# Kernel optimization log

Hardware: AMD Instinct MI355X
Metric: run time of the kernel (lower is better)

Reference implementation:

```python
import jax, jax.numpy as jnp
import numpy as np

B, N, C, R, E = 8, 4096, 128, 16, 65536


def setup_inputs() -> dict:
    key = jax.random.key(0)
    ks = jax.random.split(key, 8)
    node_features = jax.random.normal(ks[0], (B, N, C), dtype=jnp.float32)
    edge_index = jax.random.randint(ks[1], (B, 2, E), 0, N, dtype=jnp.int64)
    edge_type = jax.random.randint(ks[2], (B, E), 0, R, dtype=jnp.int64)
    s = 1.0 / np.sqrt(C)
    rel_weight = jax.random.uniform(ks[3], (R, C, C), jnp.float32, -s, s)
    root_weight = jax.random.uniform(ks[4], (C, C), jnp.float32, -s, s)
    rgcn_bias = jnp.zeros((C,), jnp.float32)
    lin_weight = jax.random.uniform(ks[5], (C, 1), jnp.float32, -s, s)
    lin_bias = jnp.zeros((1,), jnp.float32)
    return {
        'node_features': node_features,
        'edge_index': edge_index,
        'edge_type': edge_type,
        'rel_weight': rel_weight,
        'root_weight': root_weight,
        'rgcn_bias': rgcn_bias,
        'lin_weight': lin_weight,
        'lin_bias': lin_bias,
    }


def _rgcn_score(node_features, edge_index, edge_type, rel_weight, root_weight,
                rgcn_bias, lin_weight, lin_bias):
    # Flatten batch of graphs into one big disjoint graph (as batch_rgcn does).
    x = node_features.reshape(B * N, C)
    offs = (jnp.arange(B, dtype=edge_index.dtype) * N)[:, None, None]  # (B,1,1)
    ei = (edge_index + offs).transpose(1, 0, 2).reshape(2, B * E)  # (2, B*E)
    et = edge_type.reshape(B * E)
    src, dst = ei[0], ei[1]

    x_src = x[src]  # (B*E, C) gathered source features
    # root transform + bias (RGCNConv root_weight + bias)
    out = x @ root_weight + rgcn_bias  # (B*N, C)
    # per-relation mean aggregation; mean(W_r x_j) == W_r mean(x_j)
    for r in range(R):
        mask = (et == r).astype(x.dtype)  # (B*E,)
        s = jax.ops.segment_sum(x_src * mask[:, None], dst, num_segments=B * N)
        cnt = jax.ops.segment_sum(mask, dst, num_segments=B * N)
        mean = jnp.where(cnt[:, None] > 0, s / jnp.maximum(cnt, 1.0)[:, None], 0.0)
        out = out + mean @ rel_weight[r]

    out = jax.nn.relu(out)  # dropout is identity at eval
    scores = (out @ lin_weight + lin_bias).reshape(B, N)
    return scores


def reference(node_features, edge_index, edge_type, rel_weight, root_weight,
              rgcn_bias, lin_weight, lin_bias):
    return _rgcn_score(node_features, edge_index, edge_type, rel_weight,
                       root_weight, rgcn_bias, lin_weight, lin_bias)
```

## Files before the change

kernel.cpp:

```cpp
#include <hip/hip_runtime.h>

#define BB 8
#define NN 4096
#define CC 128
#define RR 16
#define EE 65536
#define NNODES 32768
#define NEDGES 524288
#define KTOT   2176
#define LDP    80
#define CSP    136
#define BCAP   60
#define GEMMB  4352
#define EDGEB  2048

typedef unsigned short ushort_t;
typedef short bf16x8 __attribute__((ext_vector_type(8)));
typedef float f32x4 __attribute__((ext_vector_type(4)));

__device__ __forceinline__ unsigned short f2b(float f) {
    unsigned u = __builtin_bit_cast(unsigned, f);
    unsigned r = (u + 0x7fffu + ((u >> 16) & 1u)) >> 16;
    return (unsigned short)r;
}
__device__ __forceinline__ float b2f(unsigned short s) {
    return __builtin_bit_cast(float, (unsigned)s << 16);
}
__device__ __forceinline__ float ldf(const void* p, int j, int isbf) {
    return isbf ? b2f(((const ushort_t*)p)[j]) : ((const float*)p)[j];
}
__device__ __forceinline__ int ldi(const int* p, int j, int is64) {
    return p[j << is64];
}

__device__ __forceinline__ int probe_isbf(const ushort_t* xf) {
    int t = threadIdx.x & 63;
    int bad = 0;
    for (int j = t; j < 512; j += 64) {
        unsigned e = (xf[j] >> 7) & 0xffu;
        if (e >= 160u) bad = 1;
    }
    return __ballot(bad) == 0ull;
}

__global__ __launch_bounds__(256) void prep_k(const void* __restrict__ x,
                                              const void* __restrict__ relw,
                                              const void* __restrict__ rootw,
                                              const int* __restrict__ ei,
                                              const int* __restrict__ et,
                                              ushort_t* __restrict__ Xb,
                                              ushort_t* __restrict__ WT,
                                              int* __restrict__ dcnt,
                                              int* __restrict__ flags) {
    int bx = blockIdx.x, t = threadIdx.x;
    if (bx < 2048) {
        int isbf = probe_isbf((const ushort_t*)x);
        int tid = bx * 256 + t;
        if (isbf) {
            ((uint4*)Xb)[tid] = ((const uint4*)x)[tid];
        } else {
            const float4* xf = (const float4*)x;
            float4 a = xf[2 * tid], b = xf[2 * tid + 1];
            ushort4 o0, o1;
            o0.x = f2b(a.x); o0.y = f2b(a.y); o0.z = f2b(a.z); o0.w = f2b(a.w);
            o1.x = f2b(b.x); o1.y = f2b(b.y); o1.z = f2b(b.z); o1.w = f2b(b.w);
            ((ushort4*)Xb)[2 * tid] = o0; ((ushort4*)Xb)[2 * tid + 1] = o1;
        }
    } else if (bx < 3136) {
        int isbf = probe_isbf((const ushort_t*)x);
        int tid = (bx - 2048) * 256 + t;
        int nglob = tid >> 7, k = tid & 127;
        int jb = nglob >> 7, n = nglob & 127;
        float v = (jb == 0) ? ldf(rootw, k * 128 + n, isbf)
                            : ldf(relw, ((jb - 1) << 14) + k * 128 + n, isbf);
        WT[tid] = f2b(v);
    } else if (bx < 3168) {
        int tid = (bx - 3136) * 256 + t;
        ((uint4*)dcnt)[tid] = make_uint4(0, 0, 0, 0);
    } else {
        if (t < 64) {
            int isbf = probe_isbf((const ushort_t*)x);
            int a = (t < 16) ? ei[2 * t + 1] : 0;
            int b = (t < 16) ? et[2 * t + 1] : 0;
            unsigned long long ma = __ballot(a != 0);
            unsigned long long mb = __ballot(b != 0);
            if (t == 0) {
                flags[0] = isbf;
                flags[1] = (ma == 0ull);
                flags[2] = (mb == 0ull);
            }
        }
    }
}

__global__ __launch_bounds__(256) void ge_k(const ushort_t* __restrict__ Xb,
                                            const ushort_t* __restrict__ WT,
                                            ushort_t* __restrict__ Y,
                                            const int* __restrict__ ei,
                                            const int* __restrict__ et,
                                            int* __restrict__ dcnt,
                                            int* __restrict__ bucket,
                                            const int* __restrict__ flags) {
    __shared__ ushort_t smem[2 * 128 * LDP];
    int bx = blockIdx.x, t = threadIdx.x;
    if (bx < EDGEB) {
        int w64i = flags[1], w64t = flags[2];
        int tid = bx * 256 + t;
        int b = tid >> 16, e = tid & 65535;
        int src = ldi(ei, (b * 2) * EE + e, w64i);
        int dst = ldi(ei, (b * 2 + 1) * EE + e, w64i);
        int r = ldi(et, tid, w64t);
        int gd = (b << 12) + dst;
        int pos = atomicAdd(&dcnt[gd], 1);
        if (pos < BCAP)
            bucket[gd * BCAP + pos] = (((b << 12) + src) << 4) | r;
        return;
    }
    int bxg = bx - EDGEB;
    ushort_t* As = smem;
    ushort_t* Bs = smem + 128 * LDP;
    int m0 = (bxg & 255) * 128, n0 = (bxg >> 8) * 128;
    int wave = t >> 6, lane = t & 63, lrow = lane & 15, lq = lane >> 4;
    int wm = (wave >> 1) * 64, wn = (wave & 1) * 64;
    f32x4 acc[4][4] = {};

    for (int kt = 0; kt < 2; ++kt) {
        #pragma unroll
        for (int i = 0; i < 4; ++i) {
            int c = t + i * 256;
            int row = c >> 3, c8 = c & 7;
            uint4 va = *(const uint4*)(Xb + (size_t)(m0 + row) * 128 + kt * 64 + c8 * 8);
            *(uint4*)(&As[row * LDP + c8 * 8]) = va;
            uint4 vb = *(const uint4*)(WT + (size_t)(n0 + row) * 128 + kt * 64 + c8 * 8);
            *(uint4*)(&Bs[row * LDP + c8 * 8]) = vb;
        }
        __syncthreads();
        #pragma unroll
        for (int ks = 0; ks < 2; ++ks) {
            int k0 = ks * 32 + lq * 8;
            bf16x8 a[4], b[4];
            #pragma unroll
            for (int mi = 0; mi < 4; ++mi) a[mi] = *(const bf16x8*)(&As[(wm + mi * 16 + lrow) * LDP + k0]);
            #pragma unroll
            for (int ni = 0; ni < 4; ++ni) b[ni] = *(const bf16x8*)(&Bs[(wn + ni * 16 + lrow) * LDP + k0]);
            #pragma unroll
            for (int mi = 0; mi < 4; ++mi)
                #pragma unroll
                for (int ni = 0; ni < 4; ++ni)
                    acc[mi][ni] = __builtin_amdgcn_mfma_f32_16x16x32_bf16(a[mi], b[ni], acc[mi][ni], 0, 0, 0);
        }
        __syncthreads();
    }
    ushort_t* Cs = smem;
    #pragma unroll
    for (int mi = 0; mi < 4; ++mi)
        #pragma unroll
        for (int rg = 0; rg < 4; ++rg) {
            int row = wm + mi * 16 + lq * 4 + rg;
            #pragma unroll
            for (int ni = 0; ni < 4; ++ni)
                Cs[row * CSP + wn + ni * 16 + lrow] = f2b(acc[mi][ni][rg]);
        }
    __syncthreads();
    #pragma unroll
    for (int i = 0; i < 8; ++i) {
        int c = t + i * 256;
        int row = c >> 4, c16 = c & 15;
        uint4 v = *(const uint4*)(&Cs[row * CSP + c16 * 8]);
        *(uint4*)(Y + (size_t)(m0 + row) * KTOT + n0 + c16 * 8) = v;
    }
}

__global__ __launch_bounds__(128) void agg_score_k(const ushort_t* __restrict__ Y,
                                                   const int* __restrict__ dcnt,
                                                   const int* __restrict__ bucket,
                                                   const void* __restrict__ bias,
                                                   const void* __restrict__ linw,
                                                   const void* __restrict__ linb,
                                                   void* __restrict__ out,
                                                   const int* __restrict__ flags) {
    int i = blockIdx.x, t = threadIdx.x;
    int isbf = flags[0];
    __shared__ int scnt[RR];
    __shared__ float inv[RR];
    __shared__ int bke[64];
    __shared__ float part[128][9];
    int nc = dcnt[i]; if (nc > BCAP) nc = BCAP;
    const int* bk = bucket + i * BCAP;
    if (t < RR) scnt[t] = 0;
    __syncthreads();
    if (t < nc) { int v = bk[t]; bke[t] = v; atomicAdd(&scnt[v & 15], 1); }
    __syncthreads();
    if (t < RR) inv[t] = (scnt[t] > 0) ? 1.0f / (float)scnt[t] : 0.0f;
    __syncthreads();

    int g = t >> 4, l16 = t & 15;
    float a8[8] = {};
    for (int base = 0; base < nc; base += 8) {
        int e = base + g;
        if (e < nc) {
            int v = bke[e];
            const ushort_t* yr = Y + (size_t)(v >> 4) * KTOT + CC + ((v & 15) << 7) + l16 * 8;
            uint4 u = *(const uint4*)yr;
            float w = inv[v & 15];
            a8[0] += w * __builtin_bit_cast(float, u.x << 16);
            a8[1] += w * __builtin_bit_cast(float, u.x & 0xffff0000u);
            a8[2] += w * __builtin_bit_cast(float, u.y << 16);
            a8[3] += w * __builtin_bit_cast(float, u.y & 0xffff0000u);
            a8[4] += w * __builtin_bit_cast(float, u.z << 16);
            a8[5] += w * __builtin_bit_cast(float, u.z & 0xffff0000u);
            a8[6] += w * __builtin_bit_cast(float, u.w << 16);
            a8[7] += w * __builtin_bit_cast(float, u.w & 0xffff0000u);
        }
    }
    #pragma unroll
    for (int j = 0; j < 8; ++j) part[l16 * 8 + j][g] = a8[j];
    __syncthreads();

    float acc = b2f(Y[(size_t)i * KTOT + t]) + ldf(bias, t, isbf);
    #pragma unroll
    for (int gg = 0; gg < 8; ++gg) acc += part[t][gg];
    float val = fmaxf(acc, 0.f) * ldf(linw, t, isbf);
    for (int o = 32; o > 0; o >>= 1) val += __shfl_down(val, o, 64);
    __shared__ float red[2];
    if ((t & 63) == 0) red[t >> 6] = val;
    __syncthreads();
    if (t == 0) {
        float res = red[0] + red[1] + ldf(linb, 0, isbf);
        if (isbf) ((ushort_t*)out)[i] = f2b(res);
        else      ((float*)out)[i] = res;
    }
}

extern "C" void kernel_launch(void* const* d_in, const int* in_sizes, int n_in,
                              void* d_out, int out_size, void* d_ws, size_t ws_size,
                              hipStream_t stream) {
    const void* x     = d_in[0];
    const int*  ei    = (const int*)d_in[1];
    const int*  et    = (const int*)d_in[2];
    const void* relw  = d_in[3];
    const void* rootw = d_in[4];
    const void* bias  = d_in[5];
    const void* linw  = d_in[6];
    const void* linb  = d_in[7];

    const size_t WS_NEED = 159547904;
    if (ws_size < WS_NEED) return;

    char* ws = (char*)d_ws;
    ushort_t* Y      = (ushort_t*)(ws);
    ushort_t* Xb     = (ushort_t*)(ws + 142606336);
    ushort_t* WT     = (ushort_t*)(ws + 150994944);
    int*      dcnt   = (int*)(ws + 151552000);
    int*      bucket = (int*)(ws + 151683072);
    int*      flags  = (int*)(ws + 159547392);

    prep_k<<<3169, 256, 0, stream>>>(x, relw, rootw, ei, et, Xb, WT, dcnt, flags);
    ge_k<<<EDGEB + GEMMB, 256, 0, stream>>>(Xb, WT, Y, ei, et, dcnt, bucket, flags);
    agg_score_k<<<NNODES, 128, 0, stream>>>(Y, dcnt, bucket, bias, linw, linb, d_out, flags);
}
```

Measured before the change: 167.1 us.

## Aggregate per relation first, then fuse concatenated GEMM with scoring

The algorithm changes from transform-then-gather to gather-then-transform. Before, a large Y = X·[root|W_r] table (32768×2176 bf16) was materialised and then gathered per edge. Now edges are bucketed by (dst, relation), and per-relation means of raw bf16 features are built in LDS for a 64-node tile. Those means are multiplied against a concatenated K=2176 weight with MFMA, and ReLU plus the linear score are fused into the epilogue. This removes the ~140MB Y write and re-read. The cost is a serial 17-pass loop per block, only 512 blocks, weights streamed straight from global memory, and a per-(node,relation) bucket capacity of 16 that could drop edges.

```diff
diff --git a/kernel.cpp b/kernel.cpp
--- a/kernel.cpp
+++ b/kernel.cpp
@@ -7,12 +7,10 @@
 #define EE 65536
 #define NNODES 32768
 #define NEDGES 524288
-#define KTOT   2176
-#define LDP    80
-#define CSP    136
-#define BCAP   60
-#define GEMMB  4352
-#define EDGEB  2048
+#define KW    2176
+#define SCAP  16
+#define NT    64
+#define ALP   136
 
 typedef unsigned short ushort_t;
 typedef short bf16x8 __attribute__((ext_vector_type(8)));
@@ -49,13 +47,28 @@
                                               const int* __restrict__ ei,
                                               const int* __restrict__ et,
                                               ushort_t* __restrict__ Xb,
-                                              ushort_t* __restrict__ WT,
-                                              int* __restrict__ dcnt,
+                                              ushort_t* __restrict__ WT2,
+                                              int* __restrict__ dcnt2,
+                                              int* __restrict__ bucket2,
                                               int* __restrict__ flags) {
     int bx = blockIdx.x, t = threadIdx.x;
     if (bx < 2048) {
+        int lane = t & 63;
+        int pa = (lane < 16) ? ei[2 * lane + 1] : 0;
+        int pb = (lane < 16) ? et[2 * lane + 1] : 0;
+        int w64i = (__ballot(pa != 0) == 0ull);
+        int w64t = (__ballot(pb != 0) == 0ull);
+        int tid = bx * 256 + t;
+        int b = tid >> 16, e = tid & 65535;
+        int src = ldi(ei, (b * 2) * EE + e, w64i);
+        int dst = ldi(ei, (b * 2 + 1) * EE + e, w64i);
+        int r = ldi(et, tid, w64t);
+        int key = (((b << 12) + dst) << 4) | r;
+        int pos = atomicAdd(&dcnt2[key], 1);
+        if (pos < SCAP) bucket2[key * SCAP + pos] = (b << 12) + src;
+    } else if (bx < 4096) {
         int isbf = probe_isbf((const ushort_t*)x);
-        int tid = bx * 256 + t;
+        int tid = (bx - 2048) * 256 + t;
         if (isbf) {
             ((uint4*)Xb)[tid] = ((const uint4*)x)[tid];
         } else {
@@ -66,169 +79,123 @@
             o1.x = f2b(b.x); o1.y = f2b(b.y); o1.z = f2b(b.z); o1.w = f2b(b.w);
             ((ushort4*)Xb)[2 * tid] = o0; ((ushort4*)Xb)[2 * tid + 1] = o1;
         }
-    } else if (bx < 3136) {
+    } else if (bx < 5184) {
         int isbf = probe_isbf((const ushort_t*)x);
-        int tid = (bx - 2048) * 256 + t;
-        int nglob = tid >> 7, k = tid & 127;
-        int jb = nglob >> 7, n = nglob & 127;
-        float v = (jb == 0) ? ldf(rootw, k * 128 + n, isbf)
-                            : ldf(relw, ((jb - 1) << 14) + k * 128 + n, isbf);
-        WT[tid] = f2b(v);
-    } else if (bx < 3168) {
-        int tid = (bx - 3136) * 256 + t;
-        ((uint4*)dcnt)[tid] = make_uint4(0, 0, 0, 0);
+        int tid = (bx - 4096) * 256 + t;
+        if (tid < 262144) {
+            int c = tid >> 11, kk = tid & 2047;
+            int r = kk >> 7, k = kk & 127;
+            WT2[c * KW + kk] = f2b(ldf(relw, (r << 14) + (k << 7) + c, isbf));
+        } else {
+            int t2 = tid - 262144;
+            int c = t2 >> 7, k = t2 & 127;
+            WT2[c * KW + 2048 + k] = f2b(ldf(rootw, (k << 7) + c, isbf));
+        }
     } else {
-        if (t < 64) {
-            int isbf = probe_isbf((const ushort_t*)x);
-            int a = (t < 16) ? ei[2 * t + 1] : 0;
-            int b = (t < 16) ? et[2 * t + 1] : 0;
-            unsigned long long ma = __ballot(a != 0);
-            unsigned long long mb = __ballot(b != 0);
-            if (t == 0) {
-                flags[0] = isbf;
-                flags[1] = (ma == 0ull);
-                flags[2] = (mb == 0ull);
+        int isbf = probe_isbf((const ushort_t*)x);
+        if (t == 0) flags[0] = isbf;
+    }
+}
+
+__global__ __launch_bounds__(256) void agg_k(const ushort_t* __restrict__ Xb,
+                                             const ushort_t* __restrict__ WT2,
+                                             const int* __restrict__ dcnt2,
+                                             const int* __restrict__ bucket2,
+                                             const void* __restrict__ bias,
+                                             const void* __restrict__ linw,
+                                             const void* __restrict__ linb,
+                                             void* __restrict__ out,
+                                             const int* __restrict__ flags) {
+    __shared__ ushort_t A[NT * ALP];
+    __shared__ int cnt[NT * 16];
+    __shared__ float red[NT][5];
+    int bx = blockIdx.x, t = threadIdx.x;
+    int isbf = flags[0];
+    int n0 = bx * NT;
+
+    #pragma unroll
+    for (int i = 0; i < 4; ++i) cnt[i * 256 + t] = dcnt2[n0 * 16 + i * 256 + t];
+
+    int nsub = t >> 2, tsub = t & 3;
+    int wave = t >> 6, lane = t & 63, lrow = lane & 15, lq = lane >> 4;
+    f32x4 acc[4][2] = {};
+
+    for (int pass = 0; pass < 17; ++pass) {
+        __syncthreads();
+        if (pass == 16) {
+            const uint4* s4 = (const uint4*)(Xb + (size_t)(n0 + nsub) * 128 + tsub * 32);
+            uint4* d4 = (uint4*)(&A[nsub * ALP + tsub * 32]);
+            #pragma unroll
+            for (int i = 0; i < 4; ++i) d4[i] = s4[i];
+        } else {
+            int cfull = cnt[nsub * 16 + pass];
+            int ce = cfull > SCAP ? SCAP : cfull;
+            float s[32];
+            #pragma unroll
+            for (int j = 0; j < 32; ++j) s[j] = 0.f;
+            const int* bk = bucket2 + ((size_t)(n0 + nsub) * 16 + pass) * SCAP;
+            for (int e2 = 0; e2 < ce; ++e2) {
+                int gs = bk[e2];
+                const unsigned* xr = (const unsigned*)(Xb + (size_t)gs * 128 + tsub * 32);
+                #pragma unroll
+                for (int j = 0; j < 16; ++j) {
+                    unsigned u = xr[j];
+                    s[2 * j]     += __builtin_bit_cast(float, u << 16);
+                    s[2 * j + 1] += __builtin_bit_cast(float, u & 0xffff0000u);
+                }
             }
-        }
-    }
-}
-
-__global__ __launch_bounds__(256) void ge_k(const ushort_t* __restrict__ Xb,
-                                            const ushort_t* __restrict__ WT,
-                                            ushort_t* __restrict__ Y,
-                                            const int* __restrict__ ei,
-                                            const int* __restrict__ et,
-                                            int* __restrict__ dcnt,
-                                            int* __restrict__ bucket,
-                                            const int* __restrict__ flags) {
-    __shared__ ushort_t smem[2 * 128 * LDP];
-    int bx = blockIdx.x, t = threadIdx.x;
-    if (bx < EDGEB) {
-        int w64i = flags[1], w64t = flags[2];
-        int tid = bx * 256 + t;
-        int b = tid >> 16, e = tid & 65535;
-        int src = ldi(ei, (b * 2) * EE + e, w64i);
-        int dst = ldi(ei, (b * 2 + 1) * EE + e, w64i);
-        int r = ldi(et, tid, w64t);
-        int gd = (b << 12) + dst;
-        int pos = atomicAdd(&dcnt[gd], 1);
-        if (pos < BCAP)
-            bucket[gd * BCAP + pos] = (((b << 12) + src) << 4) | r;
-        return;
-    }
-    int bxg = bx - EDGEB;
-    ushort_t* As = smem;
-    ushort_t* Bs = smem + 128 * LDP;
-    int m0 = (bxg & 255) * 128, n0 = (bxg >> 8) * 128;
-    int wave = t >> 6, lane = t & 63, lrow = lane & 15, lq = lane >> 4;
-    int wm = (wave >> 1) * 64, wn = (wave & 1) * 64;
-    f32x4 acc[4][4] = {};
-
-    for (int kt = 0; kt < 2; ++kt) {
+            float w = (cfull > 0) ? 1.0f / (float)cfull : 0.f;
+            uint4* d4 = (uint4*)(&A[nsub * ALP + tsub * 32]);
+            #pragma unroll
+            for (int i = 0; i < 4; ++i) {
+                uint4 v;
+                unsigned q0 = (unsigned)f2b(s[i * 8 + 0] * w) | ((unsigned)f2b(s[i * 8 + 1] * w) << 16);
+                unsigned q1 = (unsigned)f2b(s[i * 8 + 2] * w) | ((unsigned)f2b(s[i * 8 + 3] * w) << 16);
+                unsigned q2 = (unsigned)f2b(s[i * 8 + 4] * w) | ((unsigned)f2b(s[i * 8 + 5] * w) << 16);
+                unsigned q3 = (unsigned)f2b(s[i * 8 + 6] * w) | ((unsigned)f2b(s[i * 8 + 7] * w) << 16);
+                v.x = q0; v.y = q1; v.z = q2; v.w = q3;
+                d4[i] = v;
+            }
+        }
+        __syncthreads();
+        const ushort_t* bp0 = WT2 + (size_t)((wave * 2) * 16 + lrow) * KW + pass * 128;
+        const ushort_t* bp1 = bp0 + (size_t)16 * KW;
         #pragma unroll
-        for (int i = 0; i < 4; ++i) {
-            int c = t + i * 256;
-            int row = c >> 3, c8 = c & 7;
-            uint4 va = *(const uint4*)(Xb + (size_t)(m0 + row) * 128 + kt * 64 + c8 * 8);
-            *(uint4*)(&As[row * LDP + c8 * 8]) = va;
-            uint4 vb = *(const uint4*)(WT + (size_t)(n0 + row) * 128 + kt * 64 + c8 * 8);
-            *(uint4*)(&Bs[row * LDP + c8 * 8]) = vb;
-        }
-        __syncthreads();
-        #pragma unroll
-        for (int ks = 0; ks < 2; ++ks) {
+        for (int ks = 0; ks < 4; ++ks) {
             int k0 = ks * 32 + lq * 8;
-            bf16x8 a[4], b[4];
-            #pragma unroll
-            for (int mi = 0; mi < 4; ++mi) a[mi] = *(const bf16x8*)(&As[(wm + mi * 16 + lrow) * LDP + k0]);
-            #pragma unroll
-            for (int ni = 0; ni < 4; ++ni) b[ni] = *(const bf16x8*)(&Bs[(wn + ni * 16 + lrow) * LDP + k0]);
+            bf16x8 a[4], b0, b1;
             #pragma unroll
             for (int mi = 0; mi < 4; ++mi)
-                #pragma unroll
-                for (int ni = 0; ni < 4; ++ni)
-                    acc[mi][ni] = __builtin_amdgcn_mfma_f32_16x16x32_bf16(a[mi], b[ni], acc[mi][ni], 0, 0, 0);
-        }
-        __syncthreads();
-    }
-    ushort_t* Cs = smem;
+                a[mi] = *(const bf16x8*)(&A[(mi * 16 + lrow) * ALP + k0]);
+            b0 = *(const bf16x8*)(bp0 + k0);
+            b1 = *(const bf16x8*)(bp1 + k0);
+            #pragma unroll
+            for (int mi = 0; mi < 4; ++mi) {
+                acc[mi][0] = __builtin_amdgcn_mfma_f32_16x16x32_bf16(a[mi], b0, acc[mi][0], 0, 0, 0);
+                acc[mi][1] = __builtin_amdgcn_mfma_f32_16x16x32_bf16(a[mi], b1, acc[mi][1], 0, 0, 0);
+            }
+        }
+    }
+    int c0 = (wave * 2) * 16 + lrow, c1 = c0 + 16;
+    float bi0 = ldf(bias, c0, isbf), bi1 = ldf(bias, c1, isbf);
+    float lw0 = ldf(linw, c0, isbf), lw1 = ldf(linw, c1, isbf);
     #pragma unroll
     for (int mi = 0; mi < 4; ++mi)
         #pragma unroll
         for (int rg = 0; rg < 4; ++rg) {
-            int row = wm + mi * 16 + lq * 4 + rg;
-            #pragma unroll
-            for (int ni = 0; ni < 4; ++ni)
-                Cs[row * CSP + wn + ni * 16 + lrow] = f2b(acc[mi][ni][rg]);
+            float p = fmaxf(acc[mi][0][rg] + bi0, 0.f) * lw0
+                    + fmaxf(acc[mi][1][rg] + bi1, 0.f) * lw1;
+            p += __shfl_xor(p, 1, 64);
+            p += __shfl_xor(p, 2, 64);
+            p += __shfl_xor(p, 4, 64);
+            p += __shfl_xor(p, 8, 64);
+            if (lrow == 0) red[mi * 16 + lq * 4 + rg][wave] = p;
         }
     __syncthreads();
-    #pragma unroll
-    for (int i = 0; i < 8; ++i) {
-        int c = t + i * 256;
-        int row = c >> 4, c16 = c & 15;
-        uint4 v = *(const uint4*)(&Cs[row * CSP + c16 * 8]);
-        *(uint4*)(Y + (size_t)(m0 + row) * KTOT + n0 + c16 * 8) = v;
-    }
-}
-
-__global__ __launch_bounds__(128) void agg_score_k(const ushort_t* __restrict__ Y,
-                                                   const int* __restrict__ dcnt,
-                                                   const int* __restrict__ bucket,
-                                                   const void* __restrict__ bias,
-                                                   const void* __restrict__ linw,
-                                                   const void* __restrict__ linb,
-                                                   void* __restrict__ out,
-                                                   const int* __restrict__ flags) {
-    int i = blockIdx.x, t = threadIdx.x;
-    int isbf = flags[0];
-    __shared__ int scnt[RR];
-    __shared__ float inv[RR];
-    __shared__ int bke[64];
-    __shared__ float part[128][9];
-    int nc = dcnt[i]; if (nc > BCAP) nc = BCAP;
-    const int* bk = bucket + i * BCAP;
-    if (t < RR) scnt[t] = 0;
-    __syncthreads();
-    if (t < nc) { int v = bk[t]; bke[t] = v; atomicAdd(&scnt[v & 15], 1); }
-    __syncthreads();
-    if (t < RR) inv[t] = (scnt[t] > 0) ? 1.0f / (float)scnt[t] : 0.0f;
-    __syncthreads();
-
-    int g = t >> 4, l16 = t & 15;
-    float a8[8] = {};
-    for (int base = 0; base < nc; base += 8) {
-        int e = base + g;
-        if (e < nc) {
-            int v = bke[e];
-            const ushort_t* yr = Y + (size_t)(v >> 4) * KTOT + CC + ((v & 15) << 7) + l16 * 8;
-            uint4 u = *(const uint4*)yr;
-            float w = inv[v & 15];
-            a8[0] += w * __builtin_bit_cast(float, u.x << 16);
-            a8[1] += w * __builtin_bit_cast(float, u.x & 0xffff0000u);
-            a8[2] += w * __builtin_bit_cast(float, u.y << 16);
-            a8[3] += w * __builtin_bit_cast(float, u.y & 0xffff0000u);
-            a8[4] += w * __builtin_bit_cast(float, u.z << 16);
-            a8[5] += w * __builtin_bit_cast(float, u.z & 0xffff0000u);
-            a8[6] += w * __builtin_bit_cast(float, u.w << 16);
-            a8[7] += w * __builtin_bit_cast(float, u.w & 0xffff0000u);
-        }
-    }
-    #pragma unroll
-    for (int j = 0; j < 8; ++j) part[l16 * 8 + j][g] = a8[j];
-    __syncthreads();
-
-    float acc = b2f(Y[(size_t)i * KTOT + t]) + ldf(bias, t, isbf);
-    #pragma unroll
-    for (int gg = 0; gg < 8; ++gg) acc += part[t][gg];
-    float val = fmaxf(acc, 0.f) * ldf(linw, t, isbf);
-    for (int o = 32; o > 0; o >>= 1) val += __shfl_down(val, o, 64);
-    __shared__ float red[2];
-    if ((t & 63) == 0) red[t >> 6] = val;
-    __syncthreads();
-    if (t == 0) {
-        float res = red[0] + red[1] + ldf(linb, 0, isbf);
-        if (isbf) ((ushort_t*)out)[i] = f2b(res);
-        else      ((float*)out)[i] = res;
+    if (t < NT) {
+        float res = red[t][0] + red[t][1] + red[t][2] + red[t][3] + ldf(linb, 0, isbf);
+        if (isbf) ((ushort_t*)out)[n0 + t] = f2b(res);
+        else      ((float*)out)[n0 + t] = res;
     }
 }
 
@@ -244,18 +211,17 @@
     const void* linw  = d_in[6];
     const void* linb  = d_in[7];
 
-    const size_t WS_NEED = 159547904;
+    const size_t WS_NEED = 44597504;
     if (ws_size < WS_NEED) return;
 
     char* ws = (char*)d_ws;
-    ushort_t* Y      = (ushort_t*)(ws);
-    ushort_t* Xb     = (ushort_t*)(ws + 142606336);
-    ushort_t* WT     = (ushort_t*)(ws + 150994944);
-    int*      dcnt   = (int*)(ws + 151552000);
-    int*      bucket = (int*)(ws + 151683072);
-    int*      flags  = (int*)(ws + 159547392);
-
-    prep_k<<<3169, 256, 0, stream>>>(x, relw, rootw, ei, et, Xb, WT, dcnt, flags);
-    ge_k<<<EDGEB + GEMMB, 256, 0, stream>>>(Xb, WT, Y, ei, et, dcnt, bucket, flags);
-    agg_score_k<<<NNODES, 128, 0, stream>>>(Y, dcnt, bucket, bias, linw, linb, d_out, flags);
-}
+    ushort_t* Xb      = (ushort_t*)(ws);
+    ushort_t* WT2     = (ushort_t*)(ws + 8388608);
+    int*      dcnt2   = (int*)(ws + 8945664);
+    int*      bucket2 = (int*)(ws + 11042816);
+    int*      flags   = (int*)(ws + 44597248);
+
+    hipMemsetAsync(dcnt2, 0, 2097152, stream);
+    prep_k<<<5185, 256, 0, stream>>>(x, relw, rootw, ei, et, Xb, WT2, dcnt2, bucket2, flags);
+    agg_k<<<512, 256, 0, stream>>>(Xb, WT2, dcnt2, bucket2, bias, linw, linb, d_out, flags);
+}
```

Result: slower. 196.0 us (+17.3%).
